# Performance work log

Hardware: AMD Instinct MI355X
Metric: run time of the kernel (lower is better)

Reference implementation:

```python
import jax, jax.numpy as jnp
import numpy as np

D_MODEL = 1024
D_STATE = 64
D_CONV = 4
EXPAND = 2
INNER = EXPAND * D_STATE          # 128
PROJ = D_STATE + 2 * INNER        # 320
B, L = 8, 4096
EPS = 1e-4


def setup_inputs() -> dict:
    key = jax.random.key(0)
    ks = jax.random.split(key, 6)
    x = jax.random.normal(ks[0], (B, L, D_MODEL), dtype=jnp.float32)
    # depthwise conv weight, torch layout (out=D, in/group=1, K)
    conv_w = jax.random.normal(ks[1], (D_MODEL, 1, D_CONV), dtype=jnp.float32) / np.sqrt(D_CONV)
    conv_b = jnp.zeros((D_MODEL,), dtype=jnp.float32)
    in_proj_w = jax.random.normal(ks[2], (PROJ, D_MODEL), dtype=jnp.float32) / np.sqrt(D_MODEL)
    in_proj_b = jnp.zeros((PROJ,), dtype=jnp.float32)
    A_log = jax.random.normal(ks[3], (D_STATE,), dtype=jnp.float32) * 0.1
    out_proj_w = jax.random.normal(ks[4], (D_MODEL, D_STATE), dtype=jnp.float32) / np.sqrt(D_STATE)
    out_proj_b = jnp.zeros((D_MODEL,), dtype=jnp.float32)
    return {"x": x, "conv_w": conv_w, "conv_b": conv_b,
            "in_proj_w": in_proj_w, "in_proj_b": in_proj_b,
            "A_log": A_log, "out_proj_w": out_proj_w, "out_proj_b": out_proj_b}


def _ssm_forward(x, conv_w, conv_b, in_proj_w, in_proj_b, A_log, out_proj_w, out_proj_b):
    bsz, L_in, _ = x.shape
    # depthwise conv1d, padding (D_CONV-1)//2 on both sides (torch semantics)
    pad = (D_CONV - 1) // 2
    xc = jnp.transpose(x, (0, 2, 1))  # (B, D, L)
    xc = jax.lax.conv_general_dilated(
        xc, conv_w, window_strides=(1,), padding=[(pad, pad)],
        dimension_numbers=("NCH", "OIH", "NCH"), feature_group_count=D_MODEL)
    xc = xc + conv_b[None, :, None]
    Lc = xc.shape[2]
    if Lc < L_in:  # K even -> conv output is L-1; pad zeros on the right
        xc = jnp.pad(xc, ((0, 0), (0, 0), (0, L_in - Lc)))
    elif Lc > L_in:
        xc = xc[:, :, :L_in]
    xc = jnp.transpose(xc, (0, 2, 1))  # (B, L, D)

    proj = xc @ in_proj_w.T + in_proj_b  # (B, L, PROJ)
    delta = proj[..., :D_STATE]                                  # (B, L, N)
    B_in = proj[..., D_STATE:D_STATE + INNER]
    C = proj[..., D_STATE + INNER:]
    n_groups = INNER // D_STATE
    B_in = B_in.reshape(bsz, L_in, D_STATE, n_groups).mean(axis=-1)  # (B, L, N)
    C = C.reshape(bsz, L_in, D_STATE, n_groups).mean(axis=-1)        # (B, L, N)

    # ZOH discretization
    A = -jnp.exp(A_log)[None, None, :]          # (1, 1, N)
    delta = jax.nn.softplus(delta)
    dA = delta * A
    A_bar = jnp.exp(dA)                         # (B, L, N)
    A_safe = jnp.where(jnp.abs(A) < EPS, EPS * jnp.sign(A) + EPS, A)
    scale = (A_bar - 1.0) / A_safe
    taylor = 1.0 + dA / 2.0 + dA * dA / 6.0
    scale = jnp.where(jnp.abs(A) < EPS, taylor, scale)
    B_bar = scale * B_in                        # (B, L, N)

    # linear recurrence h_t = A_bar_t * h_{t-1} + B_bar_t via associative scan
    def comb(e1, e2):
        a1, b1 = e1
        a2, b2 = e2
        return a1 * a2, a2 * b1 + b2
    _, h = jax.lax.associative_scan(comb, (A_bar, B_bar), axis=1)  # (B, L, N)

    y_state = C * h
    return y_state @ out_proj_w.T + out_proj_b  # (B, L, D)


def reference(x, conv_w, conv_b, in_proj_w, in_proj_b, A_log, out_proj_w, out_proj_b):
    return _ssm_forward(x, conv_w, conv_b, in_proj_w, in_proj_b, A_log, out_proj_w, out_proj_b)
```

## Files before the change

kernel.cpp:

```cpp
#include <hip/hip_runtime.h>
#include <cstdint>
#include <cstddef>

typedef __bf16 bf16;
typedef __attribute__((ext_vector_type(4))) __bf16 bf16x4;
typedef __attribute__((ext_vector_type(8))) __bf16 bf16x8;
typedef __attribute__((ext_vector_type(4))) float f32x4;
typedef __attribute__((ext_vector_type(2))) _Float16 f16x2;

#define EPS_C 1e-4f
#define SWZ(r) (((r) ^ ((r) >> 2)) & 3)

#define BAR_LDS() do { asm volatile("s_waitcnt lgkmcnt(0)" ::: "memory"); \
                       __builtin_amdgcn_s_barrier(); } while (0)

__global__ __launch_bounds__(256) void k0_prep(const float* __restrict__ Wi,
    const float* __restrict__ Wo, bf16* __restrict__ Whg, bf16* __restrict__ Wlg,
    bf16* __restrict__ Wob, float* __restrict__ zpg)
{
    int idx = blockIdx.x * 256 + threadIdx.x;
    if (idx < 196608) {
        int nn = idx >> 10, k = idx & 1023;
        int wn = nn / 48, s = nn - wn * 48;
        if (s < 16) {
            int d = wn * 16 + s;
            float w = Wi[d * 1024 + k];
            bf16 h = (bf16)w;
            Whg[(k >> 5) * 6144 + nn * 32 + (k & 31)] = h;
            Wlg[(k >> 5) * 2048 + d * 32 + (k & 31)] = (bf16)(w - (float)h);
        } else if (s < 32) {
            int i = wn * 16 + (s - 16);
            float w = 0.5f * (Wi[(64 + 2 * i) * 1024 + k] + Wi[(65 + 2 * i) * 1024 + k]);
            Whg[(k >> 5) * 6144 + nn * 32 + (k & 31)] = (bf16)w;
        } else {
            int i = wn * 16 + (s - 32);
            float w = 0.5f * (Wi[(192 + 2 * i) * 1024 + k] + Wi[(193 + 2 * i) * 1024 + k]);
            Whg[(k >> 5) * 6144 + nn * 32 + (k & 31)] = (bf16)w;
        }
    } else if (idx < 262144) {
        int j = idx - 196608;
        Wob[j] = (bf16)Wo[j];
    } else {
        int j = idx - 262144;
        if (j < 1024) zpg[j] = 0.f;
    }
}

__global__ __launch_bounds__(512) void k1_convproj(
    const float* __restrict__ x, const float* __restrict__ conv_w,
    const float* __restrict__ conv_b, const float* __restrict__ in_proj_b,
    const float* __restrict__ A_log,
    const bf16* __restrict__ Whg, const bf16* __restrict__ Wlg,
    const float* __restrict__ zpg,
    f16x2* __restrict__ YZp,
    float* __restrict__ Psum, float* __restrict__ Ssum)
{
    __shared__ char smem[61440];

    const int tid  = threadIdx.x;
    const int lane = tid & 63;
    const int wv   = tid >> 6;
    const int wt   = wv >> 2, wn = wv & 3;
    const int fr   = lane & 15, fs = lane >> 4;
    const int b    = blockIdx.x >> 5;
    const int tc   = blockIdx.x & 31;
    const int t0   = tc * 128;
    const int rot  = (blockIdx.x * 5) & 31;

    const int tp = tid >> 3, cq = tid & 7;
    const int r0 = tp * 2, r1 = r0 + 1;
    const int gt0 = t0 + r0;
    const bool zrow1 = (gt0 + 1 == 4095);
    const int woff0 = r0 * 80 + cq * 8;
    const int woff1 = r1 * 80 + cq * 8;

    int aoff[4];
#pragma unroll
    for (int mi = 0; mi < 4; ++mi) {
        int r = wt * 64 + mi * 16 + fr;
        aoff[mi] = r * 80 + fs * 16;
    }

    const float* rp[5];
#pragma unroll
    for (int dt = 0; dt < 5; ++dt) {
        int g = gt0 - 1 + dt;
        rp[dt] = (g >= 0 && g < 4096) ? (x + ((size_t)b * 4096 + g) * 1024 + cq * 4)
                                      : (zpg + cq * 4);
    }

    const size_t wfo  = (size_t)(wn * 48 + fr) * 32 + fs * 8;
    const size_t wfol = (size_t)(wn * 16 + fr) * 32 + fs * 8;

    {
        float* cwT = (float*)(smem + 40960);
        float* cbl = (float*)(smem + 57344);
        for (int p = tid; p < 1024; p += 512) {
            f32x4 w4 = *(const f32x4*)&conv_w[p * 4];
            cwT[p]        = w4.x;
            cwT[1024 + p] = w4.y;
            cwT[2048 + p] = w4.z;
            cwT[3072 + p] = w4.w;
        }
        if (tid < 256) ((f32x4*)cbl)[tid] = ((const f32x4*)conv_b)[tid];
    }

    f32x4  xr[5];
    bf16x8 wfh[3], wfl;
    f32x4  acc[4][3] = {};

    auto L = [&](int c) { return (c + rot) & 31; };

    auto fetch_x = [&](int lc) {
#pragma unroll
        for (int dt = 0; dt < 5; ++dt)
            xr[dt] = *(const f32x4*)(rp[dt] + lc * 32);
    };
    auto fetch_w = [&](int lc) {
        const bf16* ph = Whg + (size_t)lc * 6144 + wfo;
#pragma unroll
        for (int ni = 0; ni < 3; ++ni)
            wfh[ni] = *(const bf16x8*)(ph + ni * 512);
        wfl = *(const bf16x8*)(Wlg + (size_t)lc * 2048 + wfol);
    };
    auto conv = [&](int lc, int p) {
        char* xh = smem + p * 10240;
        char* xl = smem + 20480 + p * 10240;
        const float* cwT = (const float*)(smem + 40960);
        const float* cbl = (const float*)(smem + 57344);
        const int ch0 = lc * 32 + cq * 4;
        f32x4 w0 = *(const f32x4*)&cwT[ch0];
        f32x4 w1 = *(const f32x4*)&cwT[1024 + ch0];
        f32x4 w2 = *(const f32x4*)&cwT[2048 + ch0];
        f32x4 w3 = *(const f32x4*)&cwT[3072 + ch0];
        f32x4 bb = *(const f32x4*)&cbl[ch0];
        bf16x4 hi0, lo0, hi1, lo1;
#pragma unroll
        for (int j = 0; j < 4; ++j) {
            float v0 = bb[j];
            v0 = fmaf(w0[j], xr[0][j], v0);
            v0 = fmaf(w1[j], xr[1][j], v0);
            v0 = fmaf(w2[j], xr[2][j], v0);
            v0 = fmaf(w3[j], xr[3][j], v0);
            float v1 = bb[j];
            v1 = fmaf(w0[j], xr[1][j], v1);
            v1 = fmaf(w1[j], xr[2][j], v1);
            v1 = fmaf(w2[j], xr[3][j], v1);
            v1 = fmaf(w3[j], xr[4][j], v1);
            v1 = zrow1 ? 0.f : v1;
            bf16 h0 = (bf16)v0, h1 = (bf16)v1;
            hi0[j] = h0; lo0[j] = (bf16)(v0 - (float)h0);
            hi1[j] = h1; lo1[j] = (bf16)(v1 - (float)h1);
        }
        *(bf16x4*)(xh + woff0) = hi0;
        *(bf16x4*)(xh + woff1) = hi1;
        *(bf16x4*)(xl + woff0) = lo0;
        *(bf16x4*)(xl + woff1) = lo1;
    };

    fetch_x(L(0));
    fetch_w(L(0));
    __syncthreads();
    conv(L(0), 0);
    fetch_x(L(1));
    __syncthreads();

    auto body = [&](int c, int par) {
        const char* xh = smem + par * 10240;
        const char* xl = smem + 20480 + par * 10240;
        bf16x8 ah[4], al[4];
#pragma unroll
        for (int mi = 0; mi < 4; ++mi) {
            ah[mi] = *(const bf16x8*)(xh + aoff[mi]);
            al[mi] = *(const bf16x8*)(xl + aoff[mi]);
        }
        __builtin_amdgcn_s_setprio(1);
#pragma unroll
        for (int ni = 0; ni < 3; ++ni) {
            bf16x8 bh = wfh[ni];
#pragma unroll
            for (int mi = 0; mi < 4; ++mi)
                acc[mi][ni] = __builtin_amdgcn_mfma_f32_16x16x32_bf16(ah[mi], bh, acc[mi][ni], 0, 0, 0);
#pragma unroll
            for (int mi = 0; mi < 4; ++mi)
                acc[mi][ni] = __builtin_amdgcn_mfma_f32_16x16x32_bf16(al[mi], bh, acc[mi][ni], 0, 0, 0);
        }
#pragma unroll
        for (int mi = 0; mi < 4; ++mi)
            acc[mi][0] = __builtin_amdgcn_mfma_f32_16x16x32_bf16(ah[mi], wfl, acc[mi][0], 0, 0, 0);
        __builtin_amdgcn_s_setprio(0);
        if (c + 1 < 32) {
            fetch_w(L(c + 1));
            conv(L(c + 1), par ^ 1);
            if (c + 2 < 32) fetch_x(L(c + 2));
        }
        BAR_LDS();
    };

#pragma unroll 1
    for (int cc = 0; cc < 32; cc += 2) {
        body(cc,     0);
        body(cc + 1, 1);
    }

    float* res  = (float*)smem;
    float* part = (float*)(smem + 50176);
    const int i  = lane;
    const int tg = tid >> 6;
    const float A  = -expf(A_log[i]);
    const float bd = in_proj_b[i];
    const float bB = 0.5f * (in_proj_b[64 + 2 * i] + in_proj_b[65 + 2 * i]);
    const float bC = 0.5f * (in_proj_b[192 + 2 * i] + in_proj_b[193 + 2 * i]);
    const bool tiny = fabsf(A) < EPS_C;
    const int dcol = (i >> 4) * 48 + (i & 15);

#pragma unroll 1
    for (int hh = 0; hh < 2; ++hh) {
        __syncthreads();
        if (wt == hh) {
#pragma unroll
            for (int mi = 0; mi < 4; ++mi)
#pragma unroll
                for (int ni = 0; ni < 3; ++ni) {
                    int col = wn * 48 + ni * 16 + fr;
#pragma unroll
                    for (int r = 0; r < 4; ++r)
                        res[(mi * 16 + fs * 4 + r) * 196 + col] = acc[mi][ni][r];
                }
        }
        __syncthreads();
        float av[8], bv[8], cv[8];
#pragma unroll
        for (int r = 0; r < 8; ++r) {
            int t = tg * 8 + r;
            float d  = res[t * 196 + dcol] + bd;
            float Bm = res[t * 196 + dcol + 16] + bB;
            float Cm = res[t * 196 + dcol + 32] + bC;
            float delta = (d > 20.f) ? d : log1pf(expf(d));
            float dA = delta * A;
            float abar = expf(dA);
            float sc = tiny ? (1.f + dA * 0.5f + dA * dA * (1.f / 6.f)) : ((abar - 1.f) / A);
            av[r] = abar; bv[r] = sc * Bm; cv[r] = Cm;
        }
        float P = 1.f, S = 0.f;
#pragma unroll
        for (int r = 0; r < 8; ++r) { S = fmaf(av[r], S, bv[r]); P *= av[r]; }
        part[tg * 64 + i] = P;
        part[512 + tg * 64 + i] = S;
        __syncthreads();
        float h = 0.f, pp = 1.f;
#pragma unroll
        for (int g = 0; g < 7; ++g)
            if (g < tg) {
                float Pg = part[g * 64 + i], Sg = part[512 + g * 64 + i];
                h = fmaf(Pg, h, Sg);
                pp *= Pg;
            }
        size_t ob = ((size_t)b * 4096 + t0 + hh * 64 + tg * 8) * 64 + i;
#pragma unroll
        for (int r = 0; r < 8; ++r) {
            h  = fmaf(av[r], h, bv[r]);
            pp *= av[r];
            f16x2 yz;
            yz[0] = (_Float16)(cv[r] * h);
            yz[1] = (_Float16)(cv[r] * pp);
            YZp[ob + (size_t)r * 64] = yz;
        }
        if (tg == 7) {
            size_t o = ((size_t)b * 64 + tc * 2 + hh) * 64 + i;
            Psum[o] = pp;
            Ssum[o] = h;
        }
    }
}

__global__ __launch_bounds__(64) void k2_scan2(const float* __restrict__ Psum,
    const float* __restrict__ Ssum, float* __restrict__ Carry)
{
    int b = blockIdx.x, i = threadIdx.x;
    float Pv[64], Sv[64];
#pragma unroll
    for (int c = 0; c < 64; ++c) {
        size_t o = ((size_t)(b * 64) + c) * 64 + i;
        Pv[c] = Psum[o]; Sv[c] = Ssum[o];
    }
    float h = 0.f;
#pragma unroll
    for (int c = 0; c < 64; ++c) {
        size_t o = ((size_t)(b * 64) + c) * 64 + i;
        Carry[o] = h;
        h = fmaf(Pv[c], h, Sv[c]);
    }
}

__global__ __launch_bounds__(512) void k3_scan_out(
    const f16x2* __restrict__ YZp, const float* __restrict__ Carry,
    const bf16* __restrict__ Wob, const float* __restrict__ bo,
    float* __restrict__ out)
{
    __shared__ char sm3[8192];

    const int tid  = threadIdx.x;
    const int lane = tid & 63;
    const int wv   = tid >> 6;
    const int b    = blockIdx.x >> 6;
    const int ch   = blockIdx.x & 63;
    const int t0   = ch * 64;

    const int i = lane, tg = wv;
    float cr = Carry[((size_t)(b * 64) + ch) * 64 + i];
    size_t base = ((size_t)(b * 4096) + t0 + tg * 8) * 64 + i;
#pragma unroll
    for (int r = 0; r < 8; ++r) {
        f16x2 yz = YZp[base + (size_t)r * 64];
        float y = (float)yz[0] + (float)yz[1] * cr;
        int t = tg * 8 + r;
        int off = t * 128 + ((((i >> 3) ^ (t & 7)) & 7) << 4) + (i & 7) * 2;
        *(bf16*)(sm3 + off) = (bf16)y;
    }
    __syncthreads();

    const int fr = lane & 15, fs = lane >> 4;
    bf16x8 afr[4][2];
#pragma unroll
    for (int mi = 0; mi < 4; ++mi)
#pragma unroll
        for (int ks = 0; ks < 2; ++ks) {
            int row = mi * 16 + fr;
            int slot = ks * 4 + fs;
            int off = row * 128 + (((slot ^ (row & 7)) & 7) << 4);
            afr[mi][ks] = *(const bf16x8*)(sm3 + off);
        }
    const int n0 = wv * 128;
#pragma unroll
    for (int ni = 0; ni < 8; ++ni) {
        int col = n0 + ni * 16 + fr;
        bf16x8 b0 = *(const bf16x8*)(Wob + (size_t)col * 64 + fs * 8);
        bf16x8 b1 = *(const bf16x8*)(Wob + (size_t)col * 64 + 32 + fs * 8);
        float bias = bo[col];
#pragma unroll
        for (int mi = 0; mi < 4; ++mi) {
            f32x4 a = {};
            a = __builtin_amdgcn_mfma_f32_16x16x32_bf16(afr[mi][0], b0, a, 0, 0, 0);
            a = __builtin_amdgcn_mfma_f32_16x16x32_bf16(afr[mi][1], b1, a, 0, 0, 0);
#pragma unroll
            for (int r = 0; r < 4; ++r) {
                int t = mi * 16 + fs * 4 + r;
                out[((size_t)(b * 4096) + t0 + t) * 1024 + col] = a[r] + bias;
            }
        }
    }
}

extern "C" void kernel_launch(void* const* d_in, const int* in_sizes, int n_in,
                              void* d_out, int out_size, void* d_ws, size_t ws_size,
                              hipStream_t stream) {
    const float* x          = (const float*)d_in[0];
    const float* conv_w     = (const float*)d_in[1];
    const float* conv_b     = (const float*)d_in[2];
    const float* in_proj_w  = (const float*)d_in[3];
    const float* in_proj_b  = (const float*)d_in[4];
    const float* A_log      = (const float*)d_in[5];
    const float* out_proj_w = (const float*)d_in[6];
    const float* out_proj_b = (const float*)d_in[7];
    float* out = (float*)d_out;

    char* w = (char*)d_ws;
    bf16*  Whg  = (bf16*)w;
    bf16*  Wlg  = (bf16*)(w + 393216);
    bf16*  Wob  = (bf16*)(w + 524288);
    f16x2* YZp  = (f16x2*)(w + 655360);
    float* Psum = (float*)(w + 9043968);
    float* Ssum = (float*)(w + 9175040);
    float* Carry= (float*)(w + 9306112);
    float* zpg  = (float*)(w + 9437184);

    hipLaunchKernelGGL(k0_prep,     dim3(1032), dim3(256), 0, stream,
                       in_proj_w, out_proj_w, Whg, Wlg, Wob, zpg);
    hipLaunchKernelGGL(k1_convproj, dim3(256),  dim3(512), 0, stream,
                       x, conv_w, conv_b, in_proj_b, A_log, Whg, Wlg, zpg,
                       YZp, Psum, Ssum);
    hipLaunchKernelGGL(k2_scan2,    dim3(8),    dim3(64),  0, stream, Psum, Ssum, Carry);
    hipLaunchKernelGGL(k3_scan_out, dim3(512),  dim3(512), 0, stream,
                       YZp, Carry, Wob, out_proj_b, out);
}
```

Baseline: 91.16 us.

## Stage raw x tile in LDS to avoid redundant halo loads in conv

Before, each thread loaded 5 overlapping input rows straight from global memory for the depthwise conv, so every x row was fetched about 2.5 times. Now the 130-row raw tile is loaded cooperatively once per chunk (about 2 loads per thread), written to a double-buffered LDS area, and read back by the conv from LDS. The global prefetch distance grows by one chunk. In exchange, LDS use rises from about 60KB to about 97KB per block, which may lower occupancy, and each chunk gains extra LDS writes and reads.

```diff
diff --git a/kernel.cpp b/kernel.cpp
--- a/kernel.cpp
+++ b/kernel.cpp
@@ -9,7 +9,6 @@
 typedef __attribute__((ext_vector_type(2))) _Float16 f16x2;
 
 #define EPS_C 1e-4f
-#define SWZ(r) (((r) ^ ((r) >> 2)) & 3)
 
 #define BAR_LDS() do { asm volatile("s_waitcnt lgkmcnt(0)" ::: "memory"); \
                        __builtin_amdgcn_s_barrier(); } while (0)
@@ -55,7 +54,7 @@
     f16x2* __restrict__ YZp,
     float* __restrict__ Psum, float* __restrict__ Ssum)
 {
-    __shared__ char smem[61440];
+    __shared__ char smem[99328];
 
     const int tid  = threadIdx.x;
     const int lane = tid & 63;
@@ -67,12 +66,11 @@
     const int t0   = tc * 128;
     const int rot  = (blockIdx.x * 5) & 31;
 
-    const int tp = tid >> 3, cq = tid & 7;
-    const int r0 = tp * 2, r1 = r0 + 1;
-    const int gt0 = t0 + r0;
-    const bool zrow1 = (gt0 + 1 == 4095);
-    const int woff0 = r0 * 80 + cq * 8;
-    const int woff1 = r1 * 80 + cq * 8;
+    const int tp = tid >> 3, cs = tid & 7;
+    const bool zrow1 = (t0 + tp * 2 + 1 == 4095);
+    const int woff0 = (tp * 2)     * 80 + cs * 8;
+    const int woff1 = (tp * 2 + 1) * 80 + cs * 8;
+    const int rbase = tp * 2 * 144 + cs * 16;
 
     int aoff[4];
 #pragma unroll
@@ -81,20 +79,25 @@
         aoff[mi] = r * 80 + fs * 16;
     }
 
-    const float* rp[5];
-#pragma unroll
-    for (int dt = 0; dt < 5; ++dt) {
-        int g = gt0 - 1 + dt;
-        rp[dt] = (g >= 0 && g < 4096) ? (x + ((size_t)b * 4096 + g) * 1024 + cq * 4)
-                                      : (zpg + cq * 4);
-    }
+    const float* sp[3];
+    int soff[3];
+#pragma unroll
+    for (int j = 0; j < 3; ++j) {
+        int s = tid + j * 512;
+        int row = s >> 3, q = s & 7;
+        int g = t0 - 1 + row;
+        bool ok = (s < 1048) && (g >= 0) && (g < 4096);
+        sp[j]   = ok ? (x + ((size_t)b * 4096 + g) * 1024 + q * 4) : (zpg + q * 4);
+        soff[j] = row * 144 + q * 16;
+    }
+    const bool s2ok = (tid < 24);
 
     const size_t wfo  = (size_t)(wn * 48 + fr) * 32 + fs * 8;
     const size_t wfol = (size_t)(wn * 16 + fr) * 32 + fs * 8;
 
     {
-        float* cwT = (float*)(smem + 40960);
-        float* cbl = (float*)(smem + 57344);
+        float* cwT = (float*)(smem + 78848);
+        float* cbl = (float*)(smem + 95232);
         for (int p = tid; p < 1024; p += 512) {
             f32x4 w4 = *(const f32x4*)&conv_w[p * 4];
             cwT[p]        = w4.x;
@@ -105,16 +108,22 @@
         if (tid < 256) ((f32x4*)cbl)[tid] = ((const f32x4*)conv_b)[tid];
     }
 
-    f32x4  xr[5];
+    f32x4  xs[3];
     bf16x8 wfh[3], wfl;
     f32x4  acc[4][3] = {};
 
     auto L = [&](int c) { return (c + rot) & 31; };
 
     auto fetch_x = [&](int lc) {
-#pragma unroll
-        for (int dt = 0; dt < 5; ++dt)
-            xr[dt] = *(const f32x4*)(rp[dt] + lc * 32);
+        xs[0] = *(const f32x4*)(sp[0] + lc * 32);
+        xs[1] = *(const f32x4*)(sp[1] + lc * 32);
+        if (s2ok) xs[2] = *(const f32x4*)(sp[2] + lc * 32);
+    };
+    auto raw_write = [&](int c) {
+        char* rb = smem + (c & 1) * 18944;
+        *(f32x4*)(rb + soff[0]) = xs[0];
+        *(f32x4*)(rb + soff[1]) = xs[1];
+        if (s2ok) *(f32x4*)(rb + soff[2]) = xs[2];
     };
     auto fetch_w = [&](int lc) {
         const bf16* ph = Whg + (size_t)lc * 6144 + wfo;
@@ -123,12 +132,17 @@
             wfh[ni] = *(const bf16x8*)(ph + ni * 512);
         wfl = *(const bf16x8*)(Wlg + (size_t)lc * 2048 + wfol);
     };
-    auto conv = [&](int lc, int p) {
-        char* xh = smem + p * 10240;
-        char* xl = smem + 20480 + p * 10240;
-        const float* cwT = (const float*)(smem + 40960);
-        const float* cbl = (const float*)(smem + 57344);
-        const int ch0 = lc * 32 + cq * 4;
+    auto conv = [&](int c, int lc) {
+        const char* rb = smem + (c & 1) * 18944;
+        char* xh = smem + 37888 + (c & 1) * 10240;
+        char* xl = smem + 58368 + (c & 1) * 10240;
+        const float* cwT = (const float*)(smem + 78848);
+        const float* cbl = (const float*)(smem + 95232);
+        f32x4 xt[5];
+#pragma unroll
+        for (int dt = 0; dt < 5; ++dt)
+            xt[dt] = *(const f32x4*)(rb + rbase + dt * 144);
+        const int ch0 = lc * 32 + cs * 4;
         f32x4 w0 = *(const f32x4*)&cwT[ch0];
         f32x4 w1 = *(const f32x4*)&cwT[1024 + ch0];
         f32x4 w2 = *(const f32x4*)&cwT[2048 + ch0];
@@ -138,15 +152,15 @@
 #pragma unroll
         for (int j = 0; j < 4; ++j) {
             float v0 = bb[j];
-            v0 = fmaf(w0[j], xr[0][j], v0);
-            v0 = fmaf(w1[j], xr[1][j], v0);
-            v0 = fmaf(w2[j], xr[2][j], v0);
-            v0 = fmaf(w3[j], xr[3][j], v0);
+            v0 = fmaf(w0[j], xt[0][j], v0);
+            v0 = fmaf(w1[j], xt[1][j], v0);
+            v0 = fmaf(w2[j], xt[2][j], v0);
+            v0 = fmaf(w3[j], xt[3][j], v0);
             float v1 = bb[j];
-            v1 = fmaf(w0[j], xr[1][j], v1);
-            v1 = fmaf(w1[j], xr[2][j], v1);
-            v1 = fmaf(w2[j], xr[3][j], v1);
-            v1 = fmaf(w3[j], xr[4][j], v1);
+            v1 = fmaf(w0[j], xt[1][j], v1);
+            v1 = fmaf(w1[j], xt[2][j], v1);
+            v1 = fmaf(w2[j], xt[3][j], v1);
+            v1 = fmaf(w3[j], xt[4][j], v1);
             v1 = zrow1 ? 0.f : v1;
             bf16 h0 = (bf16)v0, h1 = (bf16)v1;
             hi0[j] = h0; lo0[j] = (bf16)(v0 - (float)h0);
@@ -160,14 +174,17 @@
 
     fetch_x(L(0));
     fetch_w(L(0));
-    __syncthreads();
-    conv(L(0), 0);
+    raw_write(0);
     fetch_x(L(1));
     __syncthreads();
+    conv(0, L(0));
+    raw_write(1);
+    fetch_x(L(2));
+    BAR_LDS();
 
     auto body = [&](int c, int par) {
-        const char* xh = smem + par * 10240;
-        const char* xl = smem + 20480 + par * 10240;
+        const char* xh = smem + 37888 + par * 10240;
+        const char* xl = smem + 58368 + par * 10240;
         bf16x8 ah[4], al[4];
 #pragma unroll
         for (int mi = 0; mi < 4; ++mi) {
@@ -191,8 +208,9 @@
         __builtin_amdgcn_s_setprio(0);
         if (c + 1 < 32) {
             fetch_w(L(c + 1));
-            conv(L(c + 1), par ^ 1);
-            if (c + 2 < 32) fetch_x(L(c + 2));
+            conv(c + 1, L(c + 1));
+            if (c + 2 < 32) raw_write(c + 2);
+            if (c + 3 < 32) fetch_x(L(c + 3));
         }
         BAR_LDS();
     };
```

New measurement: 91.72 us. About the same (+0.6%).

## Double conv-projection block to 1024 threads with half the M tile per wave

Applied to the files above, without the earlier changes.

The conv+in-projection kernel now launches 1024 threads (16 waves) per block instead of 512. Each wave computes 32 rows instead of 64, so each wave holds half the accumulators and A fragments. Only the first 512 threads stage the convolution into LDS. The scan epilogue is split into 16 groups of 4 timesteps, with a larger partial-sum buffer. The aim is more waves per CU to hide memory and MFMA latency, since the grid has only one block per CU. The cost is that each weight fragment is fetched by twice as many waves. The launch bound of (1024, 4) may also force a tight register budget and cause spills.

```diff
diff --git a/kernel.cpp b/kernel.cpp
--- a/kernel.cpp
+++ b/kernel.cpp
@@ -9,7 +9,6 @@
 typedef __attribute__((ext_vector_type(2))) _Float16 f16x2;
 
 #define EPS_C 1e-4f
-#define SWZ(r) (((r) ^ ((r) >> 2)) & 3)
 
 #define BAR_LDS() do { asm volatile("s_waitcnt lgkmcnt(0)" ::: "memory"); \
                        __builtin_amdgcn_s_barrier(); } while (0)
@@ -46,7 +45,7 @@
     }
 }
 
-__global__ __launch_bounds__(512) void k1_convproj(
+__global__ __launch_bounds__(1024, 4) void k1_convproj(
     const float* __restrict__ x, const float* __restrict__ conv_w,
     const float* __restrict__ conv_b, const float* __restrict__ in_proj_b,
     const float* __restrict__ A_log,
@@ -67,26 +66,25 @@
     const int t0   = tc * 128;
     const int rot  = (blockIdx.x * 5) & 31;
 
-    const int tp = tid >> 3, cq = tid & 7;
-    const int r0 = tp * 2, r1 = r0 + 1;
-    const int gt0 = t0 + r0;
-    const bool zrow1 = (gt0 + 1 == 4095);
-    const int woff0 = r0 * 80 + cq * 8;
-    const int woff1 = r1 * 80 + cq * 8;
-
-    int aoff[4];
-#pragma unroll
-    for (int mi = 0; mi < 4; ++mi) {
-        int r = wt * 64 + mi * 16 + fr;
+    const bool stg = (tid < 512);
+    const int tp = tid >> 3, cs = tid & 7;
+    const bool zrow1 = (t0 + tp * 2 + 1 == 4095);
+    const int woff0 = (tp * 2)     * 80 + cs * 8;
+    const int woff1 = (tp * 2 + 1) * 80 + cs * 8;
+
+    int aoff[2];
+#pragma unroll
+    for (int mi = 0; mi < 2; ++mi) {
+        int r = wt * 32 + mi * 16 + fr;
         aoff[mi] = r * 80 + fs * 16;
     }
 
     const float* rp[5];
 #pragma unroll
     for (int dt = 0; dt < 5; ++dt) {
-        int g = gt0 - 1 + dt;
-        rp[dt] = (g >= 0 && g < 4096) ? (x + ((size_t)b * 4096 + g) * 1024 + cq * 4)
-                                      : (zpg + cq * 4);
+        int g = t0 + tp * 2 - 1 + dt;
+        rp[dt] = (stg && g >= 0 && g < 4096) ? (x + ((size_t)b * 4096 + g) * 1024 + cs * 4)
+                                             : (zpg + cs * 4);
     }
 
     const size_t wfo  = (size_t)(wn * 48 + fr) * 32 + fs * 8;
@@ -95,7 +93,8 @@
     {
         float* cwT = (float*)(smem + 40960);
         float* cbl = (float*)(smem + 57344);
-        for (int p = tid; p < 1024; p += 512) {
+        if (tid < 1024) {
+            int p = tid;
             f32x4 w4 = *(const f32x4*)&conv_w[p * 4];
             cwT[p]        = w4.x;
             cwT[1024 + p] = w4.y;
@@ -107,14 +106,16 @@
 
     f32x4  xr[5];
     bf16x8 wfh[3], wfl;
-    f32x4  acc[4][3] = {};
+    f32x4  acc[2][3] = {};
 
     auto L = [&](int c) { return (c + rot) & 31; };
 
     auto fetch_x = [&](int lc) {
-#pragma unroll
-        for (int dt = 0; dt < 5; ++dt)
-            xr[dt] = *(const f32x4*)(rp[dt] + lc * 32);
+        if (stg) {
+#pragma unroll
+            for (int dt = 0; dt < 5; ++dt)
+                xr[dt] = *(const f32x4*)(rp[dt] + lc * 32);
+        }
     };
     auto fetch_w = [&](int lc) {
         const bf16* ph = Whg + (size_t)lc * 6144 + wfo;
@@ -128,7 +129,7 @@
         char* xl = smem + 20480 + p * 10240;
         const float* cwT = (const float*)(smem + 40960);
         const float* cbl = (const float*)(smem + 57344);
-        const int ch0 = lc * 32 + cq * 4;
+        const int ch0 = lc * 32 + cs * 4;
         f32x4 w0 = *(const f32x4*)&cwT[ch0];
         f32x4 w1 = *(const f32x4*)&cwT[1024 + ch0];
         f32x4 w2 = *(const f32x4*)&cwT[2048 + ch0];
@@ -161,16 +162,16 @@
     fetch_x(L(0));
     fetch_w(L(0));
     __syncthreads();
-    conv(L(0), 0);
+    if (stg) conv(L(0), 0);
     fetch_x(L(1));
-    __syncthreads();
+    BAR_LDS();
 
     auto body = [&](int c, int par) {
         const char* xh = smem + par * 10240;
         const char* xl = smem + 20480 + par * 10240;
-        bf16x8 ah[4], al[4];
-#pragma unroll
-        for (int mi = 0; mi < 4; ++mi) {
+        bf16x8 ah[2], al[2];
+#pragma unroll
+        for (int mi = 0; mi < 2; ++mi) {
             ah[mi] = *(const bf16x8*)(xh + aoff[mi]);
             al[mi] = *(const bf16x8*)(xl + aoff[mi]);
         }
@@ -179,20 +180,22 @@
         for (int ni = 0; ni < 3; ++ni) {
             bf16x8 bh = wfh[ni];
 #pragma unroll
-            for (int mi = 0; mi < 4; ++mi)
+            for (int mi = 0; mi < 2; ++mi)
                 acc[mi][ni] = __builtin_amdgcn_mfma_f32_16x16x32_bf16(ah[mi], bh, acc[mi][ni], 0, 0, 0);
 #pragma unroll
-            for (int mi = 0; mi < 4; ++mi)
+            for (int mi = 0; mi < 2; ++mi)
                 acc[mi][ni] = __builtin_amdgcn_mfma_f32_16x16x32_bf16(al[mi], bh, acc[mi][ni], 0, 0, 0);
         }
 #pragma unroll
-        for (int mi = 0; mi < 4; ++mi)
+        for (int mi = 0; mi < 2; ++mi)
             acc[mi][0] = __builtin_amdgcn_mfma_f32_16x16x32_bf16(ah[mi], wfl, acc[mi][0], 0, 0, 0);
         __builtin_amdgcn_s_setprio(0);
         if (c + 1 < 32) {
             fetch_w(L(c + 1));
-            conv(L(c + 1), par ^ 1);
-            if (c + 2 < 32) fetch_x(L(c + 2));
+            if (stg) {
+                conv(L(c + 1), par ^ 1);
+                if (c + 2 < 32) fetch_x(L(c + 2));
+            }
         }
         BAR_LDS();
     };
@@ -217,22 +220,22 @@
 #pragma unroll 1
     for (int hh = 0; hh < 2; ++hh) {
         __syncthreads();
-        if (wt == hh) {
-#pragma unroll
-            for (int mi = 0; mi < 4; ++mi)
+        if ((wv >> 3) == hh) {
+#pragma unroll
+            for (int mi = 0; mi < 2; ++mi)
 #pragma unroll
                 for (int ni = 0; ni < 3; ++ni) {
                     int col = wn * 48 + ni * 16 + fr;
 #pragma unroll
                     for (int r = 0; r < 4; ++r)
-                        res[(mi * 16 + fs * 4 + r) * 196 + col] = acc[mi][ni][r];
+                        res[((wt & 1) * 32 + mi * 16 + fs * 4 + r) * 196 + col] = acc[mi][ni][r];
                 }
         }
         __syncthreads();
-        float av[8], bv[8], cv[8];
-#pragma unroll
-        for (int r = 0; r < 8; ++r) {
-            int t = tg * 8 + r;
+        float av[4], bv[4], cv[4];
+#pragma unroll
+        for (int r = 0; r < 4; ++r) {
+            int t = tg * 4 + r;
             float d  = res[t * 196 + dcol] + bd;
             float Bm = res[t * 196 + dcol + 16] + bB;
             float Cm = res[t * 196 + dcol + 32] + bC;
@@ -244,21 +247,21 @@
         }
         float P = 1.f, S = 0.f;
 #pragma unroll
-        for (int r = 0; r < 8; ++r) { S = fmaf(av[r], S, bv[r]); P *= av[r]; }
+        for (int r = 0; r < 4; ++r) { S = fmaf(av[r], S, bv[r]); P *= av[r]; }
         part[tg * 64 + i] = P;
-        part[512 + tg * 64 + i] = S;
+        part[1024 + tg * 64 + i] = S;
         __syncthreads();
         float h = 0.f, pp = 1.f;
 #pragma unroll
-        for (int g = 0; g < 7; ++g)
+        for (int g = 0; g < 15; ++g)
             if (g < tg) {
-                float Pg = part[g * 64 + i], Sg = part[512 + g * 64 + i];
+                float Pg = part[g * 64 + i], Sg = part[1024 + g * 64 + i];
                 h = fmaf(Pg, h, Sg);
                 pp *= Pg;
             }
-        size_t ob = ((size_t)b * 4096 + t0 + hh * 64 + tg * 8) * 64 + i;
-#pragma unroll
-        for (int r = 0; r < 8; ++r) {
+        size_t ob = ((size_t)b * 4096 + t0 + hh * 64 + tg * 4) * 64 + i;
+#pragma unroll
+        for (int r = 0; r < 4; ++r) {
             h  = fmaf(av[r], h, bv[r]);
             pp *= av[r];
             f16x2 yz;
@@ -266,7 +269,7 @@
             yz[1] = (_Float16)(cv[r] * pp);
             YZp[ob + (size_t)r * 64] = yz;
         }
-        if (tg == 7) {
+        if (tg == 15) {
             size_t o = ((size_t)b * 64 + tc * 2 + hh) * 64 + i;
             Psum[o] = pp;
             Ssum[o] = h;
@@ -377,7 +380,7 @@
 
     hipLaunchKernelGGL(k0_prep,     dim3(1032), dim3(256), 0, stream,
                        in_proj_w, out_proj_w, Whg, Wlg, Wob, zpg);
-    hipLaunchKernelGGL(k1_convproj, dim3(256),  dim3(512), 0, stream,
+    hipLaunchKernelGGL(k1_convproj, dim3(256),  dim3(1024), 0, stream,
                        x, conv_w, conv_b, in_proj_b, A_log, Whg, Wlg, zpg,
                        YZp, Psum, Ssum);
     hipLaunchKernelGGL(k2_scan2,    dim3(8),    dim3(64),  0, stream, Psum, Ssum, Carry);
```

New measurement: 98.08 us. 7.6% more time.
